# Kernel optimization log

Measured on AMD Instinct MI355X. Metric: run time of the kernel, lower is better.

## Reference

```python
import jax, jax.numpy as jnp
import numpy as np

DIM = 1024
NUM_HEADS = 16
HEAD_DIM = DIM // NUM_HEADS  # 64
WINDOW = 256
SCALE = HEAD_DIM ** -0.5


def setup_inputs() -> dict:
    key = jax.random.key(0)
    ks = jax.random.split(key, 5)
    B, L = 4, 4096
    x = jax.random.normal(ks[0], (B, L, DIM), dtype=jnp.float32)
    # Linear weights stored torch-style as (out_features, in_features)
    q_w = jax.random.normal(ks[1], (DIM, DIM), dtype=jnp.float32) * (DIM ** -0.5)
    kv_w = jax.random.normal(ks[2], (2 * HEAD_DIM, DIM), dtype=jnp.float32) * (DIM ** -0.5)
    proj_w = jax.random.normal(ks[3], (DIM, DIM), dtype=jnp.float32) * (DIM ** -0.5)
    proj_b = jax.random.normal(ks[4], (DIM,), dtype=jnp.float32) * 0.01
    return {"x": x, "q_w": q_w, "kv_w": kv_w, "proj_w": proj_w, "proj_b": proj_b}


def reference(x, q_w, kv_w, proj_w, proj_b):
    B, L, D = x.shape
    H, hd, ws = NUM_HEADS, HEAD_DIM, WINDOW
    # MQA projections
    q = x @ q_w.T                                  # (B, L, D)
    kv = x @ kv_w.T                                # (B, L, 2*hd)
    k, v = kv[..., :hd], kv[..., hd:]              # (B, L, hd) single KV head
    q = q.reshape(B, L, H, hd).transpose(0, 2, 1, 3)  # (B, H, L, hd)
    # Pad sequence to a multiple of the window size (static at trace time)
    pad = (ws - L % ws) % ws
    Lp = L + pad
    if pad > 0:
        q = jnp.pad(q, ((0, 0), (0, 0), (0, pad), (0, 0)))
        k = jnp.pad(k, ((0, 0), (0, pad), (0, 0)))
        v = jnp.pad(v, ((0, 0), (0, pad), (0, 0)))
    n = Lp // ws
    qb = q.reshape(B, H, n, ws, hd)                # (B, H, n, w, d)
    kb = k.reshape(B, n, ws, hd)                   # (B, n, w, d) broadcast over heads
    vb = v.reshape(B, n, ws, hd)
    # Dense per-window attention with MQA-aware KV broadcast (no expand)
    attn = jnp.einsum('bhnwd,bnud->bhnwu', qb, kb) * SCALE
    attn = jax.nn.softmax(attn, axis=-1)
    out = jnp.einsum('bhnwu,bnud->bhnwd', attn, vb)  # (B, H, n, w, d)
    out = out.reshape(B, H, Lp, hd)[:, :, :L, :]
    out = out.transpose(0, 2, 1, 3).reshape(B, L, D)  # b h l d -> b l (h d)
    return out @ proj_w.T + proj_b
```

## Files before the change

kernel.cpp:

```cpp
#include <hip/hip_runtime.h>

typedef short bf16x8 __attribute__((ext_vector_type(8)));
typedef float f32x4 __attribute__((ext_vector_type(4)));
typedef unsigned int u32x4 __attribute__((ext_vector_type(4)));

#define QSCALE 0.18033688011112042f

__device__ __forceinline__ unsigned short f2bf(float x) {
  unsigned int u = __float_as_uint(x);
  u = (u + 0x7FFFu + ((u >> 16) & 1u)) >> 16;
  return (unsigned short)u;
}

__device__ __forceinline__ unsigned pack_rn(float a, float b) {
  unsigned au = __float_as_uint(a) + 0x8000u;
  unsigned bu = __float_as_uint(b) + 0x8000u;
  return (bu & 0xFFFF0000u) | (au >> 16);
}

__device__ __forceinline__ void async16(const void* g, void* l) {
  typedef const __attribute__((address_space(1))) unsigned int* gp_t;
  typedef __attribute__((address_space(3))) unsigned int* lp_t;
  __builtin_amdgcn_global_load_lds((gp_t)g, (lp_t)l, 16, 0, 0);
}

union frag_u { bf16x8 f; unsigned int u[4]; };

__global__ void cast_w3(const float* __restrict__ qw, const float* __restrict__ kvw,
                        const float* __restrict__ pw, unsigned short* __restrict__ qwo,
                        unsigned short* __restrict__ kvwo, unsigned short* __restrict__ pwo) {
  int i = blockIdx.x * 256 + threadIdx.x;
  const float* src; unsigned short* dst; int j;
  if (i < 262144)      { src = qw;  dst = qwo;  j = i; }
  else if (i < 294912) { src = kvw; dst = kvwo; j = i - 262144; }
  else                 { src = pw;  dst = pwo;  j = i - 294912; }
  float4 v = ((const float4*)src)[j];
  ushort4 o;
  o.x = f2bf(v.x); o.y = f2bf(v.y); o.z = f2bf(v.z); o.w = f2bf(v.w);
  ((ushort4*)dst)[j] = o;
}

template<int MODE>
__global__ __launch_bounds__(512, 2) void gemm256(
    const unsigned short* __restrict__ A,
    const unsigned short* __restrict__ Bw,
    unsigned short* __restrict__ Cbf,
    float* __restrict__ Cf,
    const float* __restrict__ bias,
    const float oscale,
    int M, int N, int K)
{
  __shared__ unsigned short S[65536];
  const int t = threadIdx.x;
  const int lane = t & 63, wave = t >> 6;
  const int g = lane >> 4, r = lane & 15;
  const int wm = wave >> 2, wn = wave & 3;

  const int nby = N >> 8;
  const int cpx = gridDim.x >> 3;
  const int bid = blockIdx.x;
  const int swz = (bid & 7) * cpx + (bid >> 3);
  const long row0 = (long)(swz / nby) * 256;
  const long col0 = (long)(swz % nby) * 256;

  const int NT = K >> 6;

  auto stage = [&](const unsigned short* gsrc, long grow0, int kcol0, int region) {
#pragma unroll
    for (int i = 0; i < 2; ++i) {
      int o = (i * 512 + t) << 4;
      int row = o >> 7;
      int scol = (o & 127) ^ ((row & 7) << 4);
      async16(gsrc + (grow0 + row) * K + kcol0 + (scol >> 1),
              (char*)S + region + i * 8192 + wave * 1024);
    }
  };
  auto ldA = [&](int bo, int ar, int ks) {
    return *(const bf16x8*)((const char*)S + bo + ar * 128 +
                            ((ks * 64 + g * 16) ^ ((ar & 7) << 4)));
  };
  auto ldB = [&](int bo, int br, int ks) {
    return *(const bf16x8*)((const char*)S + bo + 32768 + br * 128 +
                            ((ks * 64 + g * 16) ^ ((br & 7) << 4)));
  };

  f32x4 acc[8][4] = {};
  bf16x8 aF[4][2], b01[2][2], b23[2][2];

  stage(A,  row0,       0, 0);
  stage(A,  row0 + 128, 0, 16384);
  stage(Bw, col0,       0, 32768);
  stage(Bw, col0 + 128, 0, 32768 + 16384);
  if (NT > 1) {
    stage(Bw, col0,       64, 65536 + 32768);
    stage(Bw, col0 + 128, 64, 65536 + 32768 + 16384);
    asm volatile("s_waitcnt vmcnt(4)" ::: "memory");
  } else {
    asm volatile("s_waitcnt vmcnt(0)" ::: "memory");
  }
  __builtin_amdgcn_s_barrier();

  for (int kt = 0; kt < NT; ++kt) {
    const int bo = (kt & 1) << 16;
#pragma unroll
    for (int mf = 0; mf < 4; ++mf) {
      int ar = wm * 128 + mf * 16 + r;
      aF[mf][0] = ldA(bo, ar, 0); aF[mf][1] = ldA(bo, ar, 1);
    }
#pragma unroll
    for (int nf = 0; nf < 2; ++nf) {
      int br = wn * 64 + nf * 16 + r;
      b01[nf][0] = ldB(bo, br, 0); b01[nf][1] = ldB(bo, br, 1);
    }
    if (kt + 1 < NT) stage(A, row0, (kt + 1) * 64, bo ^ 65536);
    __builtin_amdgcn_s_barrier();
    __builtin_amdgcn_s_setprio(1);
#pragma unroll
    for (int mf = 0; mf < 4; ++mf)
#pragma unroll
      for (int nf = 0; nf < 2; ++nf) {
        acc[mf][nf] = __builtin_amdgcn_mfma_f32_16x16x32_bf16(aF[mf][0], b01[nf][0], acc[mf][nf], 0, 0, 0);
        acc[mf][nf] = __builtin_amdgcn_mfma_f32_16x16x32_bf16(aF[mf][1], b01[nf][1], acc[mf][nf], 0, 0, 0);
      }
    __builtin_amdgcn_s_setprio(0);
#pragma unroll
    for (int nf = 0; nf < 2; ++nf) {
      int br = wn * 64 + (nf + 2) * 16 + r;
      b23[nf][0] = ldB(bo, br, 0); b23[nf][1] = ldB(bo, br, 1);
    }
    if (kt + 1 < NT) stage(A, row0 + 128, (kt + 1) * 64, (bo ^ 65536) + 16384);
    __builtin_amdgcn_s_barrier();
    __builtin_amdgcn_s_setprio(1);
#pragma unroll
    for (int mf = 0; mf < 4; ++mf)
#pragma unroll
      for (int nf = 0; nf < 2; ++nf) {
        acc[mf][nf + 2] = __builtin_amdgcn_mfma_f32_16x16x32_bf16(aF[mf][0], b23[nf][0], acc[mf][nf + 2], 0, 0, 0);
        acc[mf][nf + 2] = __builtin_amdgcn_mfma_f32_16x16x32_bf16(aF[mf][1], b23[nf][1], acc[mf][nf + 2], 0, 0, 0);
      }
    __builtin_amdgcn_s_setprio(0);
#pragma unroll
    for (int mf = 0; mf < 4; ++mf) {
      int ar = wm * 128 + (mf + 4) * 16 + r;
      aF[mf][0] = ldA(bo, ar, 0); aF[mf][1] = ldA(bo, ar, 1);
    }
    if (kt + 2 < NT) stage(Bw, col0, (kt + 2) * 64, bo + 32768);
    __builtin_amdgcn_s_barrier();
    __builtin_amdgcn_s_setprio(1);
#pragma unroll
    for (int mf = 0; mf < 4; ++mf)
#pragma unroll
      for (int nf = 0; nf < 2; ++nf) {
        acc[mf + 4][nf + 2] = __builtin_amdgcn_mfma_f32_16x16x32_bf16(aF[mf][0], b23[nf][0], acc[mf + 4][nf + 2], 0, 0, 0);
        acc[mf + 4][nf + 2] = __builtin_amdgcn_mfma_f32_16x16x32_bf16(aF[mf][1], b23[nf][1], acc[mf + 4][nf + 2], 0, 0, 0);
      }
    __builtin_amdgcn_s_setprio(0);
    if (kt + 2 < NT) stage(Bw, col0 + 128, (kt + 2) * 64, bo + 32768 + 16384);
    __builtin_amdgcn_s_setprio(1);
#pragma unroll
    for (int mf = 0; mf < 4; ++mf)
#pragma unroll
      for (int nf = 0; nf < 2; ++nf) {
        acc[mf + 4][nf] = __builtin_amdgcn_mfma_f32_16x16x32_bf16(aF[mf][0], b01[nf][0], acc[mf + 4][nf], 0, 0, 0);
        acc[mf + 4][nf] = __builtin_amdgcn_mfma_f32_16x16x32_bf16(aF[mf][1], b01[nf][1], acc[mf + 4][nf], 0, 0, 0);
      }
    __builtin_amdgcn_s_setprio(0);
    if (kt < NT - 2)      asm volatile("s_waitcnt vmcnt(4)" ::: "memory");
    else if (kt < NT - 1) asm volatile("s_waitcnt vmcnt(0)" ::: "memory");
    if (kt < NT - 1) __builtin_amdgcn_s_barrier();
  }

  if (MODE == 0) {
#pragma unroll
    for (int mf = 0; mf < 8; ++mf)
#pragma unroll
      for (int nf = 0; nf < 4; ++nf) {
        long rr = row0 + wm * 128 + mf * 16 + g * 4;
        long cc = col0 + wn * 64 + nf * 16 + r;
#pragma unroll
        for (int i = 0; i < 4; ++i)
          Cbf[(rr + i) * N + cc] = f2bf(acc[mf][nf][i] * oscale);
      }
  } else {
#pragma unroll
    for (int mf = 0; mf < 8; ++mf)
#pragma unroll
      for (int nf = 0; nf < 4; ++nf) {
        long rr = row0 + wm * 128 + mf * 16 + g * 4;
        long cc = col0 + wn * 64 + nf * 16 + r;
        float bb = bias[cc];
#pragma unroll
        for (int i = 0; i < 4; ++i)
          Cf[(rr + i) * N + cc] = acc[mf][nf][i] + bb;
      }
  }
}

__global__ __launch_bounds__(256) void gemm_kv_cast(
    const float* __restrict__ x,
    const unsigned short* __restrict__ Bw,
    unsigned short* __restrict__ xbf,
    unsigned short* __restrict__ Kout,
    unsigned short* __restrict__ VTout)
{
  __shared__ unsigned short As[64 * 64];
  __shared__ unsigned short Bs[128 * 64];
  const int t = threadIdx.x;
  const int lane = t & 63, wave = t >> 6;
  const int g = lane >> 4, r = lane & 15;
  const int wr = wave >> 1, wc = wave & 1;
  const long row0 = (long)blockIdx.x * 64;
  const int arow = t >> 2, aq = t & 3;

  f32x4 acc[2][4] = {};

  for (int kt = 0; kt < 1024; kt += 64) {
    __syncthreads();
    float4 av[4];
    const float4* src = (const float4*)(x + (row0 + arow) * 1024 + kt + aq * 16);
#pragma unroll
    for (int i = 0; i < 4; ++i) av[i] = src[i];
#pragma unroll
    for (int i = 0; i < 4; ++i) {
      int o = (i * 256 + t) << 4;
      int brow = o >> 7;
      int scol = (o & 127) ^ ((brow & 7) << 4);
      async16(Bw + brow * 1024 + kt + (scol >> 1), (char*)Bs + i * 4096 + wave * 1024);
    }
    u32x4 u0, u1;
    u0[0] = pack_rn(av[0].x, av[0].y); u0[1] = pack_rn(av[0].z, av[0].w);
    u0[2] = pack_rn(av[1].x, av[1].y); u0[3] = pack_rn(av[1].z, av[1].w);
    u1[0] = pack_rn(av[2].x, av[2].y); u1[1] = pack_rn(av[2].z, av[2].w);
    u1[2] = pack_rn(av[3].x, av[3].y); u1[3] = pack_rn(av[3].z, av[3].w);
    {
      char* base = (char*)As + arow * 128;
      *(u32x4*)(base + ((aq * 32) ^ ((arow & 7) << 4))) = u0;
      *(u32x4*)(base + ((aq * 32 + 16) ^ ((arow & 7) << 4))) = u1;
      char* gb = (char*)(xbf + (row0 + arow) * 1024 + kt + aq * 16);
      *(u32x4*)(gb) = u0;
      *(u32x4*)(gb + 16) = u1;
    }
    __syncthreads();
#pragma unroll
    for (int ks = 0; ks < 2; ++ks) {
      bf16x8 af[2], bfr[4];
#pragma unroll
      for (int rf = 0; rf < 2; ++rf) {
        int ar = wr * 32 + rf * 16 + r;
        af[rf] = *(const bf16x8*)((const char*)As + ar * 128 + ((ks * 64 + g * 16) ^ ((ar & 7) << 4)));
      }
#pragma unroll
      for (int cf = 0; cf < 4; ++cf) {
        int br = wc * 64 + cf * 16 + r;
        bfr[cf] = *(const bf16x8*)((const char*)Bs + br * 128 + ((ks * 64 + g * 16) ^ ((br & 7) << 4)));
      }
#pragma unroll
      for (int rf = 0; rf < 2; ++rf)
#pragma unroll
        for (int cf = 0; cf < 4; ++cf)
          acc[rf][cf] = __builtin_amdgcn_mfma_f32_16x16x32_bf16(af[rf], bfr[cf], acc[rf][cf], 0, 0, 0);
    }
  }

  if (wc == 0) {
#pragma unroll
    for (int rf = 0; rf < 2; ++rf)
#pragma unroll
      for (int cf = 0; cf < 4; ++cf) {
        long rr = row0 + wr * 32 + rf * 16 + g * 4;
        int cc = cf * 16 + r;
#pragma unroll
        for (int i = 0; i < 4; ++i)
          Kout[(rr + i) * 64 + cc] = f2bf(acc[rf][cf][i]);
      }
  } else {
#pragma unroll
    for (int rf = 0; rf < 2; ++rf)
#pragma unroll
      for (int cf = 0; cf < 4; ++cf) {
        long tok = row0 + wr * 32 + rf * 16 + g * 4;
        long w16 = tok >> 8;
        int kp = (int)(tok & 255);
        int hd = cf * 16 + r;
        ushort4 pk;
        pk.x = f2bf(acc[rf][cf][0]); pk.y = f2bf(acc[rf][cf][1]);
        pk.z = f2bf(acc[rf][cf][2]); pk.w = f2bf(acc[rf][cf][3]);
        *(ushort4*)(VTout + (w16 * 64 + hd) * 256 + kp) = pk;
      }
  }
}

__global__ __launch_bounds__(512, 2) void attn_win(
    const unsigned short* __restrict__ qb,
    const unsigned short* __restrict__ kb,
    const unsigned short* __restrict__ vt,
    unsigned short* __restrict__ ao)
{
  __shared__ unsigned short Ks[256 * 64];
  __shared__ unsigned short Vs[64 * 256];

  const int blk = blockIdx.x;
  const int hp = blk & 7;
  const int w16 = blk >> 3;
  const long tok0 = (long)w16 * 256;
  const int t = threadIdx.x;
  const int lane = t & 63, wave = t >> 6;
  const int g = lane >> 4, r = lane & 15;
  const int h = hp * 2 + (wave >> 2);
  const int qw = wave & 3;

#pragma unroll
  for (int i = 0; i < 4; ++i) {
    int o = (i * 512 + t) << 4;
    int row = o >> 7;
    int ph = ((row & 3) << 1) | ((row >> 3) & 1);
    int scol = (o & 127) ^ (ph << 4);
    async16(kb + (tok0 + row) * 64 + (scol >> 1), (char*)Ks + i * 8192 + wave * 1024);
  }
  const unsigned short* vbase = vt + (long)w16 * (64 * 256);
#pragma unroll
  for (int i = 0; i < 4; ++i) {
    int o = (i * 512 + t) << 4;
    int hd = o >> 9;
    int scol = (o & 511) ^ ((hd & 7) << 4);
    async16(vbase + (long)hd * 256 + (scol >> 1), (char*)Vs + i * 8192 + wave * 1024);
  }

  bf16x8 qf[4][2];
#pragma unroll
  for (int cq = 0; cq < 4; ++cq)
#pragma unroll
    for (int kh = 0; kh < 2; ++kh)
      qf[cq][kh] = *(const bf16x8*)(qb + (tok0 + qw * 64 + cq * 16 + r) * 1024 + h * 64 + kh * 32 + g * 8);

  f32x4 O[4][4] = {};
  float sp[4] = {0.f, 0.f, 0.f, 0.f};
  const int rsub = 8 * (r >> 2) + (r & 3);
  __syncthreads();

#pragma unroll
  for (int kc = 0; kc < 8; ++kc) {
    f32x4 sc[2][4] = {};
#pragma unroll
    for (int kr = 0; kr < 2; ++kr) {
      int kp = kc * 32 + kr * 4 + rsub;
      int ph = ((kp & 3) << 1) | ((kp >> 3) & 1);
      bf16x8 kf0 = *(const bf16x8*)((const char*)Ks + kp * 128 + ((g * 16) ^ (ph << 4)));
      bf16x8 kf1 = *(const bf16x8*)((const char*)Ks + kp * 128 + ((64 + g * 16) ^ (ph << 4)));
#pragma unroll
      for (int cq = 0; cq < 4; ++cq) {
        sc[kr][cq] = __builtin_amdgcn_mfma_f32_16x16x32_bf16(kf0, qf[cq][0], sc[kr][cq], 0, 0, 0);
        sc[kr][cq] = __builtin_amdgcn_mfma_f32_16x16x32_bf16(kf1, qf[cq][1], sc[kr][cq], 0, 0, 0);
      }
    }
    bf16x8 vf[4];
#pragma unroll
    for (int ch = 0; ch < 4; ++ch) {
      int hd = ch * 16 + r;
      vf[ch] = *(const bf16x8*)((const char*)Vs + hd * 512 + ((kc * 64 + g * 16) ^ ((hd & 7) << 4)));
    }
#pragma unroll
    for (int cq = 0; cq < 4; ++cq) {
#pragma unroll
      for (int kr = 0; kr < 2; ++kr)
#pragma unroll
        for (int i = 0; i < 4; ++i)
          sc[kr][cq][i] = __builtin_amdgcn_exp2f(sc[kr][cq][i]);
      sp[cq] += ((sc[0][cq][0] + sc[0][cq][1]) + (sc[0][cq][2] + sc[0][cq][3])) +
                ((sc[1][cq][0] + sc[1][cq][1]) + (sc[1][cq][2] + sc[1][cq][3]));
    }
#pragma unroll
    for (int rq = 0; rq < 4; ++rq) {
      frag_u pa;
      pa.u[0] = pack_rn(sc[0][rq][0], sc[0][rq][1]);
      pa.u[1] = pack_rn(sc[0][rq][2], sc[0][rq][3]);
      pa.u[2] = pack_rn(sc[1][rq][0], sc[1][rq][1]);
      pa.u[3] = pack_rn(sc[1][rq][2], sc[1][rq][3]);
#pragma unroll
      for (int ch = 0; ch < 4; ++ch)
        O[rq][ch] = __builtin_amdgcn_mfma_f32_16x16x32_bf16(pa.f, vf[ch], O[rq][ch], 0, 0, 0);
    }
  }
  float inv[4];
#pragma unroll
  for (int cq = 0; cq < 4; ++cq) {
    float s = sp[cq];
    s += __shfl_xor(s, 16);
    s += __shfl_xor(s, 32);
    inv[cq] = 1.0f / s;
  }
#pragma unroll
  for (int rq = 0; rq < 4; ++rq)
#pragma unroll
    for (int i = 0; i < 4; ++i) {
      float w = __shfl(inv[rq], g * 4 + i);
      long tokr = tok0 + qw * 64 + rq * 16 + g * 4 + i;
#pragma unroll
      for (int ch = 0; ch < 4; ++ch)
        ao[tokr * 1024 + h * 64 + ch * 16 + r] = f2bf(O[rq][ch][i] * w);
    }
}

extern "C" void kernel_launch(void* const* d_in, const int* in_sizes, int n_in,
                              void* d_out, int out_size, void* d_ws, size_t ws_size,
                              hipStream_t stream) {
  const float* x      = (const float*)d_in[0];
  const float* q_w    = (const float*)d_in[1];
  const float* kv_w   = (const float*)d_in[2];
  const float* proj_w = (const float*)d_in[3];
  const float* proj_b = (const float*)d_in[4];

  char* ws = (char*)d_ws;
  unsigned short* x_bf   = (unsigned short*)(ws + 0);
  unsigned short* q_bf   = (unsigned short*)(ws + 33554432);
  unsigned short* ao_bf  = (unsigned short*)(ws + 67108864);
  unsigned short* qw_bf  = (unsigned short*)(ws + 100663296);
  unsigned short* pw_bf  = (unsigned short*)(ws + 102760448);
  unsigned short* kvw_bf = (unsigned short*)(ws + 104857600);
  unsigned short* k_bf   = (unsigned short*)(ws + 105119744);
  unsigned short* vt_bf  = (unsigned short*)(ws + 107216896);
  if (ws_size < 109314048) return;

  cast_w3<<<2176, 256, 0, stream>>>(q_w, kv_w, proj_w, qw_bf, kvw_bf, pw_bf);
  gemm_kv_cast<<<256, 256, 0, stream>>>(x, kvw_bf, x_bf, k_bf, vt_bf);

  gemm256<0><<<256, 512, 0, stream>>>(x_bf, qw_bf, q_bf, nullptr, nullptr, QSCALE, 16384, 1024, 1024);
  attn_win<<<512, 512, 0, stream>>>(q_bf, k_bf, vt_bf, ao_bf);
  gemm256<1><<<256, 512, 0, stream>>>(ao_bf, pw_bf, nullptr, (float*)d_out, proj_b, 1.0f, 16384, 1024, 1024);
}
```

Measured before the change: 142.8 us.

## Shrink GEMM tile to 128x256 with K-step 32 and double the grid

Cuts the projection GEMM block tile from 256x256 with K=64 steps to 128x256 with K=32 steps, with a new LDS swizzle layout and fewer barriers per iteration. Shared memory drops from 128KB to 48KB and the grid grows from 256 to 512 blocks. The aim is to fill all CUs of the MI355X, since 256 blocks under-occupy 256 CUs with launch bounds of 2, and to allow more resident blocks. The cost is lower arithmetic intensity per tile, more global and LDS traffic, and twice as many K iterations.

```diff
diff --git a/kernel.cpp b/kernel.cpp
--- a/kernel.cpp
+++ b/kernel.cpp
@@ -50,7 +50,7 @@
     const float oscale,
     int M, int N, int K)
 {
-  __shared__ unsigned short S[65536];
+  __shared__ unsigned short S[24576];
   const int t = threadIdx.x;
   const int lane = t & 63, wave = t >> 6;
   const int g = lane >> 4, r = lane & 15;
@@ -60,122 +60,84 @@
   const int cpx = gridDim.x >> 3;
   const int bid = blockIdx.x;
   const int swz = (bid & 7) * cpx + (bid >> 3);
-  const long row0 = (long)(swz / nby) * 256;
+  const long row0 = (long)(swz / nby) * 128;
   const long col0 = (long)(swz % nby) * 256;
 
-  const int NT = K >> 6;
-
-  auto stage = [&](const unsigned short* gsrc, long grow0, int kcol0, int region) {
-#pragma unroll
-    for (int i = 0; i < 2; ++i) {
-      int o = (i * 512 + t) << 4;
-      int row = o >> 7;
-      int scol = (o & 127) ^ ((row & 7) << 4);
-      async16(gsrc + (grow0 + row) * K + kcol0 + (scol >> 1),
-              (char*)S + region + i * 8192 + wave * 1024);
-    }
+  const int NT = K >> 5;
+
+  const int so = t << 4;
+  const int rpl = so >> 7;
+  const int slr = (rpl << 1) | ((so >> 6) & 1);
+  const int scb = (so & 63) ^ ((rpl & 3) << 4);
+
+  auto stageA = [&](int kt, int region) {
+    async16(A + (row0 + slr) * K + kt * 32 + (scb >> 1),
+            (char*)S + region + (t << 4));
   };
-  auto ldA = [&](int bo, int ar, int ks) {
-    return *(const bf16x8*)((const char*)S + bo + ar * 128 +
-                            ((ks * 64 + g * 16) ^ ((ar & 7) << 4)));
+  auto stageB = [&](int kt, int region) {
+#pragma unroll
+    for (int h = 0; h < 2; ++h)
+      async16(Bw + (col0 + h * 128 + slr) * K + kt * 32 + (scb >> 1),
+              (char*)S + region + h * 8192 + (t << 4));
   };
-  auto ldB = [&](int bo, int br, int ks) {
-    return *(const bf16x8*)((const char*)S + bo + 32768 + br * 128 +
-                            ((ks * 64 + g * 16) ^ ((br & 7) << 4)));
+  auto ldA = [&](int bo, int ar) {
+    return *(const bf16x8*)((const char*)S + bo + ((ar >> 1) << 7) + ((ar & 1) << 6) +
+                            ((g << 4) ^ (((ar >> 1) & 3) << 4)));
   };
-
-  f32x4 acc[8][4] = {};
-  bf16x8 aF[4][2], b01[2][2], b23[2][2];
-
-  stage(A,  row0,       0, 0);
-  stage(A,  row0 + 128, 0, 16384);
-  stage(Bw, col0,       0, 32768);
-  stage(Bw, col0 + 128, 0, 32768 + 16384);
+  auto ldB = [&](int bo, int br) {
+    return *(const bf16x8*)((const char*)S + bo + 8192 + ((br >> 1) << 7) + ((br & 1) << 6) +
+                            ((g << 4) ^ (((br >> 1) & 3) << 4)));
+  };
+
+  f32x4 acc[4][4] = {};
+  bf16x8 aF[4], bF[4];
+
+  stageA(0, 0);
+  stageB(0, 8192);
   if (NT > 1) {
-    stage(Bw, col0,       64, 65536 + 32768);
-    stage(Bw, col0 + 128, 64, 65536 + 32768 + 16384);
-    asm volatile("s_waitcnt vmcnt(4)" ::: "memory");
+    stageB(1, 24576 + 8192);
+    asm volatile("s_waitcnt vmcnt(2)" ::: "memory");
   } else {
     asm volatile("s_waitcnt vmcnt(0)" ::: "memory");
   }
   __builtin_amdgcn_s_barrier();
 
   for (int kt = 0; kt < NT; ++kt) {
-    const int bo = (kt & 1) << 16;
-#pragma unroll
-    for (int mf = 0; mf < 4; ++mf) {
-      int ar = wm * 128 + mf * 16 + r;
-      aF[mf][0] = ldA(bo, ar, 0); aF[mf][1] = ldA(bo, ar, 1);
-    }
-#pragma unroll
-    for (int nf = 0; nf < 2; ++nf) {
-      int br = wn * 64 + nf * 16 + r;
-      b01[nf][0] = ldB(bo, br, 0); b01[nf][1] = ldB(bo, br, 1);
-    }
-    if (kt + 1 < NT) stage(A, row0, (kt + 1) * 64, bo ^ 65536);
+    const int bo = (kt & 1) * 24576;
+    if (kt + 1 < NT) stageA(kt + 1, bo ^ 24576);
+#pragma unroll
+    for (int nf = 0; nf < 4; ++nf) bF[nf] = ldB(bo, wn * 64 + nf * 16 + r);
+#pragma unroll
+    for (int mf = 0; mf < 2; ++mf) aF[mf] = ldA(bo, wm * 64 + mf * 16 + r);
+    __builtin_amdgcn_s_setprio(1);
+#pragma unroll
+    for (int mf = 0; mf < 2; ++mf)
+#pragma unroll
+      for (int nf = 0; nf < 4; ++nf)
+        acc[mf][nf] = __builtin_amdgcn_mfma_f32_16x16x32_bf16(aF[mf], bF[nf], acc[mf][nf], 0, 0, 0);
+    __builtin_amdgcn_s_setprio(0);
     __builtin_amdgcn_s_barrier();
+    if (kt + 2 < NT) stageB(kt + 2, bo + 8192);
+#pragma unroll
+    for (int mf = 2; mf < 4; ++mf) aF[mf] = ldA(bo, wm * 64 + mf * 16 + r);
     __builtin_amdgcn_s_setprio(1);
 #pragma unroll
-    for (int mf = 0; mf < 4; ++mf)
-#pragma unroll
-      for (int nf = 0; nf < 2; ++nf) {
-        acc[mf][nf] = __builtin_amdgcn_mfma_f32_16x16x32_bf16(aF[mf][0], b01[nf][0], acc[mf][nf], 0, 0, 0);
-        acc[mf][nf] = __builtin_amdgcn_mfma_f32_16x16x32_bf16(aF[mf][1], b01[nf][1], acc[mf][nf], 0, 0, 0);
-      }
+    for (int mf = 2; mf < 4; ++mf)
+#pragma unroll
+      for (int nf = 0; nf < 4; ++nf)
+        acc[mf][nf] = __builtin_amdgcn_mfma_f32_16x16x32_bf16(aF[mf], bF[nf], acc[mf][nf], 0, 0, 0);
     __builtin_amdgcn_s_setprio(0);
-#pragma unroll
-    for (int nf = 0; nf < 2; ++nf) {
-      int br = wn * 64 + (nf + 2) * 16 + r;
-      b23[nf][0] = ldB(bo, br, 0); b23[nf][1] = ldB(bo, br, 1);
-    }
-    if (kt + 1 < NT) stage(A, row0 + 128, (kt + 1) * 64, (bo ^ 65536) + 16384);
-    __builtin_amdgcn_s_barrier();
-    __builtin_amdgcn_s_setprio(1);
-#pragma unroll
-    for (int mf = 0; mf < 4; ++mf)
-#pragma unroll
-      for (int nf = 0; nf < 2; ++nf) {
-        acc[mf][nf + 2] = __builtin_amdgcn_mfma_f32_16x16x32_bf16(aF[mf][0], b23[nf][0], acc[mf][nf + 2], 0, 0, 0);
-        acc[mf][nf + 2] = __builtin_amdgcn_mfma_f32_16x16x32_bf16(aF[mf][1], b23[nf][1], acc[mf][nf + 2], 0, 0, 0);
-      }
-    __builtin_amdgcn_s_setprio(0);
-#pragma unroll
-    for (int mf = 0; mf < 4; ++mf) {
-      int ar = wm * 128 + (mf + 4) * 16 + r;
-      aF[mf][0] = ldA(bo, ar, 0); aF[mf][1] = ldA(bo, ar, 1);
-    }
-    if (kt + 2 < NT) stage(Bw, col0, (kt + 2) * 64, bo + 32768);
-    __builtin_amdgcn_s_barrier();
-    __builtin_amdgcn_s_setprio(1);
-#pragma unroll
-    for (int mf = 0; mf < 4; ++mf)
-#pragma unroll
-      for (int nf = 0; nf < 2; ++nf) {
-        acc[mf + 4][nf + 2] = __builtin_amdgcn_mfma_f32_16x16x32_bf16(aF[mf][0], b23[nf][0], acc[mf + 4][nf + 2], 0, 0, 0);
-        acc[mf + 4][nf + 2] = __builtin_amdgcn_mfma_f32_16x16x32_bf16(aF[mf][1], b23[nf][1], acc[mf + 4][nf + 2], 0, 0, 0);
-      }
-    __builtin_amdgcn_s_setprio(0);
-    if (kt + 2 < NT) stage(Bw, col0 + 128, (kt + 2) * 64, bo + 32768 + 16384);
-    __builtin_amdgcn_s_setprio(1);
-#pragma unroll
-    for (int mf = 0; mf < 4; ++mf)
-#pragma unroll
-      for (int nf = 0; nf < 2; ++nf) {
-        acc[mf + 4][nf] = __builtin_amdgcn_mfma_f32_16x16x32_bf16(aF[mf][0], b01[nf][0], acc[mf + 4][nf], 0, 0, 0);
-        acc[mf + 4][nf] = __builtin_amdgcn_mfma_f32_16x16x32_bf16(aF[mf][1], b01[nf][1], acc[mf + 4][nf], 0, 0, 0);
-      }
-    __builtin_amdgcn_s_setprio(0);
-    if (kt < NT - 2)      asm volatile("s_waitcnt vmcnt(4)" ::: "memory");
+    if (kt < NT - 2)      asm volatile("s_waitcnt vmcnt(2)" ::: "memory");
     else if (kt < NT - 1) asm volatile("s_waitcnt vmcnt(0)" ::: "memory");
     if (kt < NT - 1) __builtin_amdgcn_s_barrier();
   }
 
   if (MODE == 0) {
 #pragma unroll
-    for (int mf = 0; mf < 8; ++mf)
+    for (int mf = 0; mf < 4; ++mf)
 #pragma unroll
       for (int nf = 0; nf < 4; ++nf) {
-        long rr = row0 + wm * 128 + mf * 16 + g * 4;
+        long rr = row0 + wm * 64 + mf * 16 + g * 4;
         long cc = col0 + wn * 64 + nf * 16 + r;
 #pragma unroll
         for (int i = 0; i < 4; ++i)
@@ -183,10 +145,10 @@
       }
   } else {
 #pragma unroll
-    for (int mf = 0; mf < 8; ++mf)
+    for (int mf = 0; mf < 4; ++mf)
 #pragma unroll
       for (int nf = 0; nf < 4; ++nf) {
-        long rr = row0 + wm * 128 + mf * 16 + g * 4;
+        long rr = row0 + wm * 64 + mf * 16 + g * 4;
         long cc = col0 + wn * 64 + nf * 16 + r;
         float bb = bias[cc];
 #pragma unroll
@@ -424,7 +386,7 @@
   cast_w3<<<2176, 256, 0, stream>>>(q_w, kv_w, proj_w, qw_bf, kvw_bf, pw_bf);
   gemm_kv_cast<<<256, 256, 0, stream>>>(x, kvw_bf, x_bf, k_bf, vt_bf);
 
-  gemm256<0><<<256, 512, 0, stream>>>(x_bf, qw_bf, q_bf, nullptr, nullptr, QSCALE, 16384, 1024, 1024);
+  gemm256<0><<<512, 512, 0, stream>>>(x_bf, qw_bf, q_bf, nullptr, nullptr, QSCALE, 16384, 1024, 1024);
   attn_win<<<512, 512, 0, stream>>>(q_bf, k_bf, vt_bf, ao_bf);
-  gemm256<1><<<256, 512, 0, stream>>>(ao_bf, pw_bf, nullptr, (float*)d_out, proj_b, 1.0f, 16384, 1024, 1024);
-}
+  gemm256<1><<<512, 512, 0, stream>>>(ao_bf, pw_bf, nullptr, (float*)d_out, proj_b, 1.0f, 16384, 1024, 1024);
+}
```

After: 148.7 us. 1.04x slower.
